# Optimization experiments

Measured on AMD Instinct MI355X. Metric: run time of the kernel, lower is better.

## Reference

```python
import jax, jax.numpy as jnp
import numpy as np

FEAT_DIM = 2048
NUM_CLASSES = 1000
BATCH = 8192
REACH_SCALE = 10.0
COS_SCALE = 16.0


def setup_inputs() -> dict:
    key = jax.random.key(0)
    ks = jax.random.split(key, 7)
    x = jax.random.normal(ks[0], (BATCH, FEAT_DIM), dtype=jnp.float32)
    centroids = jax.random.normal(ks[1], (NUM_CLASSES, FEAT_DIM), dtype=jnp.float32)
    # nn.Linear-style params (W: [out, in], b: [out]), small init scale
    s_h = 1.0 / np.sqrt(FEAT_DIM)
    W_hall = jax.random.uniform(ks[2], (NUM_CLASSES, FEAT_DIM), jnp.float32, -s_h, s_h)
    b_hall = jax.random.uniform(ks[3], (NUM_CLASSES,), jnp.float32, -s_h, s_h)
    W_sel = jax.random.uniform(ks[4], (FEAT_DIM, FEAT_DIM), jnp.float32, -s_h, s_h)
    b_sel = jax.random.uniform(ks[5], (FEAT_DIM,), jnp.float32, -s_h, s_h)
    # CosNorm_Classifier weight: [num_classes, feat_dim]
    W_cos = jax.random.uniform(ks[6], (NUM_CLASSES, FEAT_DIM), jnp.float32, -s_h, s_h)
    return {"x": x, "centroids": centroids, "W_hall": W_hall, "b_hall": b_hall,
            "W_sel": W_sel, "b_sel": b_sel, "W_cos": W_cos}


def reference(x, centroids, W_hall, b_hall, W_sel, b_sel, W_cos):
    # --- min Euclidean distance to centroids via the matmul identity ---
    x_sq = jnp.sum(x * x, axis=1, keepdims=True)               # [B, 1]
    c_sq = jnp.sum(centroids * centroids, axis=1)[None, :]     # [1, C]
    d2 = x_sq + c_sq - 2.0 * (x @ centroids.T)                 # [B, C]
    min_dist = jnp.sqrt(jnp.maximum(jnp.min(d2, axis=1), 0.0)) # [B]
    reachability = (REACH_SCALE / min_dist)[:, None]           # [B, 1] (broadcasts over feat)

    # --- hallucinated memory attention over class centroids ---
    values_memory = jax.nn.softmax(x @ W_hall.T + b_hall, axis=1)  # [B, C]
    memory_feature = values_memory @ centroids                     # [B, D]

    # --- gated fusion ---
    concept_selector = jnp.tanh(x @ W_sel.T + b_sel)               # [B, D]
    infused_feature = concept_selector * memory_feature            # [B, D]
    fused = reachability * (x + infused_feature)                   # [B, D]

    # --- CosNorm classifier: scale * (|x|/(1+|x|)) * (x/|x|) @ (W/|W|)^T ---
    norm_x = jnp.linalg.norm(fused, axis=1, keepdims=True)         # [B, 1]
    ex = (norm_x / (1.0 + norm_x)) * (fused / norm_x)              # [B, D]
    ew = W_cos / jnp.linalg.norm(W_cos, axis=1, keepdims=True)     # [C, D]
    logits = COS_SCALE * (ex @ ew.T)                               # [B, C]

    direct_feature = x
    return logits, direct_feature, infused_feature
```

## Files before the change

kernel.cpp:

```cpp
#include <hip/hip_runtime.h>
#include <hip/hip_bf16.h>

typedef __bf16 bf16x8 __attribute__((ext_vector_type(8)));
typedef float  f32x4  __attribute__((ext_vector_type(4)));
typedef unsigned short u16;

__device__ __forceinline__ u16 f2bf(float f) {
    __hip_bfloat16 h = __float2bfloat16(f);
    return __builtin_bit_cast(unsigned short, h);
}
__device__ __forceinline__ float bf2f(u16 u) {
    return __bfloat162float(__builtin_bit_cast(__hip_bfloat16, u));
}

template <int MODE>
__device__ __forceinline__ float blockReduce(float v, float* sbuf) {
    #pragma unroll
    for (int off = 32; off > 0; off >>= 1) {
        float o = __shfl_down(v, off, 64);
        v = (MODE == 0) ? v + o : (MODE == 1) ? fmaxf(v, o) : fminf(v, o);
    }
    int lane = threadIdx.x & 63, w = threadIdx.x >> 6;
    __syncthreads();
    if (lane == 0) sbuf[w] = v;
    __syncthreads();
    float r = sbuf[0];
    #pragma unroll
    for (int i = 1; i < 4; ++i) {
        float o = sbuf[i];
        r = (MODE == 0) ? r + o : (MODE == 1) ? fmaxf(r, o) : fminf(r, o);
    }
    return r;
}

__global__ void convert_x(const float* __restrict__ src, u16* __restrict__ dst,
                          float* __restrict__ rowsq, float* __restrict__ copyOut) {
    __shared__ float sbuf[4];
    int r = blockIdx.x, t = threadIdx.x;
    size_t base = (size_t)r * 2048 + t * 8;
    float4 a0 = *(const float4*)(src + base);
    float4 a1 = *(const float4*)(src + base + 4);
    float ss = a0.x*a0.x + a0.y*a0.y + a0.z*a0.z + a0.w*a0.w
             + a1.x*a1.x + a1.y*a1.y + a1.z*a1.z + a1.w*a1.w;
    ushort4 u0, u1;
    u0.x = f2bf(a0.x); u0.y = f2bf(a0.y); u0.z = f2bf(a0.z); u0.w = f2bf(a0.w);
    u1.x = f2bf(a1.x); u1.y = f2bf(a1.y); u1.z = f2bf(a1.z); u1.w = f2bf(a1.w);
    *(ushort4*)(dst + base)     = u0;
    *(ushort4*)(dst + base + 4) = u1;
    *(float4*)(copyOut + base)     = a0;
    *(float4*)(copyOut + base + 4) = a1;
    ss = blockReduce<0>(ss, sbuf);
    if (t == 0) rowsq[r] = ss;
}

__global__ void convert_weights(const float* __restrict__ cent, const float* __restrict__ whall,
                                const float* __restrict__ wsel, u16* __restrict__ Bp,
                                float* __restrict__ csq) {
    __shared__ float sbuf[4];
    int r = blockIdx.x, t = threadIdx.x;
    const float* src; int sr; bool valid;
    if (r < 1024)       { src = cent;  sr = r;        valid = sr < 1000; }
    else if (r < 2048)  { src = whall; sr = r - 1024; valid = sr < 1000; }
    else                { src = wsel;  sr = r - 2048; valid = true; }
    size_t dbase = (size_t)r * 2048 + t * 8;
    float ss = 0.f;
    ushort4 u0 = {0,0,0,0}, u1 = {0,0,0,0};
    if (valid) {
        size_t sbase = (size_t)sr * 2048 + t * 8;
        float4 a0 = *(const float4*)(src + sbase);
        float4 a1 = *(const float4*)(src + sbase + 4);
        ss = a0.x*a0.x + a0.y*a0.y + a0.z*a0.z + a0.w*a0.w
           + a1.x*a1.x + a1.y*a1.y + a1.z*a1.z + a1.w*a1.w;
        u0.x = f2bf(a0.x); u0.y = f2bf(a0.y); u0.z = f2bf(a0.z); u0.w = f2bf(a0.w);
        u1.x = f2bf(a1.x); u1.y = f2bf(a1.y); u1.z = f2bf(a1.z); u1.w = f2bf(a1.w);
    }
    *(ushort4*)(Bp + dbase)     = u0;
    *(ushort4*)(Bp + dbase + 4) = u1;
    if (r < 1024) {
        ss = blockReduce<0>(ss, sbuf);
        if (t == 0) csq[r] = ss;
    }
}

__global__ void norm_rows(const float* __restrict__ src, u16* __restrict__ dst, int validRows) {
    __shared__ float sbuf[4];
    int r = blockIdx.x, t = threadIdx.x;
    size_t base = (size_t)r * 2048 + t * 8;
    ushort4 u0 = {0,0,0,0}, u1 = {0,0,0,0};
    if (r < validRows) {
        float4 a0 = *(const float4*)(src + base);
        float4 a1 = *(const float4*)(src + base + 4);
        float ss = a0.x*a0.x + a0.y*a0.y + a0.z*a0.z + a0.w*a0.w
                 + a1.x*a1.x + a1.y*a1.y + a1.z*a1.z + a1.w*a1.w;
        ss = blockReduce<0>(ss, sbuf);
        float sc = 1.f / sqrtf(ss);
        u0.x = f2bf(a0.x*sc); u0.y = f2bf(a0.y*sc); u0.z = f2bf(a0.z*sc); u0.w = f2bf(a0.w*sc);
        u1.x = f2bf(a1.x*sc); u1.y = f2bf(a1.y*sc); u1.z = f2bf(a1.z*sc); u1.w = f2bf(a1.w*sc);
    }
    *(ushort4*)(dst + base)     = u0;
    *(ushort4*)(dst + base + 4) = u1;
}

__global__ void transpose_to_bf16(const float* __restrict__ src, u16* __restrict__ dst, int validRows) {
    __shared__ u16 tile[32][33];
    int d0 = blockIdx.x * 32;
    int c0 = blockIdx.y * 32;
    int tx = threadIdx.x, ty = threadIdx.y;
    #pragma unroll
    for (int k = 0; k < 4; ++k) {
        int c = c0 + ty + k * 8;
        float v = (c < validRows) ? src[(size_t)c * 2048 + d0 + tx] : 0.f;
        tile[ty + k * 8][tx] = f2bf(v);
    }
    __syncthreads();
    #pragma unroll
    for (int k = 0; k < 4; ++k) {
        int d = d0 + ty + k * 8;
        dst[(size_t)d * 1024 + c0 + tx] = tile[tx][ty + k * 8];
    }
}

template <int EPI>
__global__ __launch_bounds__(256, 4)
void gemm_bt(const u16* __restrict__ A, const u16* __restrict__ Bt,
             float* __restrict__ Cf, u16* __restrict__ Cb,
             int K, int ldc, int nValid,
             const float* __restrict__ bias,
             const u16* __restrict__ selp, int ldsel,
             const float* __restrict__ reach, const u16* __restrict__ xh2,
             u16* __restrict__ fusedh) {
    __shared__ u16 As[128 * 64];
    __shared__ u16 Bs[128 * 64];
    const int tid  = threadIdx.x;
    const int lane = tid & 63;
    const int w    = tid >> 6;
    const int wr   = w >> 1, wc = w & 1;
    const int quad = lane >> 4, r16 = lane & 15;
    const int sw   = r16 & 7;
    const int lr   = lane >> 3;
    const int lc   = lane & 7;
    const int lk   = (lc ^ lr) * 8;
    const size_t rowBase = (size_t)blockIdx.y * 128;
    const size_t colBase = (size_t)blockIdx.x * 128;

    f32x4 acc[4][4] = {};

    for (int kt = 0; kt < K; kt += 64) {
        #pragma unroll
        for (int i = 0; i < 4; ++i) {
            int ci = w * 4 + i;
            const u16* ga = A  + (rowBase + ci * 8 + lr) * (size_t)K + kt + lk;
            const u16* gb = Bt + (colBase + ci * 8 + lr) * (size_t)K + kt + lk;
            __builtin_amdgcn_global_load_lds(
                (const __attribute__((address_space(1))) void*)ga,
                (__attribute__((address_space(3))) void*)(As + ci * 512), 16, 0, 0);
            __builtin_amdgcn_global_load_lds(
                (const __attribute__((address_space(1))) void*)gb,
                (__attribute__((address_space(3))) void*)(Bs + ci * 512), 16, 0, 0);
        }
        __syncthreads();
        #pragma unroll
        for (int kk2 = 0; kk2 < 2; ++kk2) {
            const int off = (((kk2 << 2) | quad) ^ sw) * 8;
            bf16x8 a[4], b[4];
            #pragma unroll
            for (int i = 0; i < 4; ++i)
                a[i] = *(const bf16x8*)(As + (wr * 64 + i * 16 + r16) * 64 + off);
            #pragma unroll
            for (int j = 0; j < 4; ++j)
                b[j] = *(const bf16x8*)(Bs + (wc * 64 + j * 16 + r16) * 64 + off);
            #pragma unroll
            for (int i = 0; i < 4; ++i)
                #pragma unroll
                for (int j = 0; j < 4; ++j)
                    acc[i][j] = __builtin_amdgcn_mfma_f32_16x16x32_bf16(a[i], b[j], acc[i][j], 0, 0, 0);
        }
        __syncthreads();
    }

    #pragma unroll
    for (int i = 0; i < 4; ++i) {
        #pragma unroll
        for (int j = 0; j < 4; ++j) {
            #pragma unroll
            for (int v = 0; v < 4; ++v) {
                size_t grow = rowBase + wr * 64 + i * 16 + quad * 4 + v;
                size_t gcol = colBase + wc * 64 + j * 16 + r16;
                float val = acc[i][j][v];
                if (EPI == 1) {
                    Cb[grow * (size_t)ldc + gcol] = f2bf(val);
                } else if (EPI == 2) {
                    float sv  = bf2f(selp[grow * (size_t)ldsel + gcol]);
                    float t   = tanhf(sv + bias[gcol]);
                    float inf = t * val;
                    Cf[grow * (size_t)ldc + gcol] = inf;
                    float xv = bf2f(xh2[grow * (size_t)ldc + gcol]);
                    fusedh[grow * (size_t)ldc + gcol] = f2bf(reach[grow] * (xv + inf));
                } else if (EPI == 3) {
                    if ((int)gcol < nValid) Cf[grow * (size_t)ldc + gcol] = bias[grow] * val;
                }
            }
        }
    }
}

__global__ void min_softmax(const u16* __restrict__ Sp, const float* __restrict__ xsq,
                            const float* __restrict__ csq, const float* __restrict__ bh,
                            float* __restrict__ reach, u16* __restrict__ Vm) {
    __shared__ float sbuf[4];
    int r = blockIdx.x, t = threadIdx.x;
    size_t rb = (size_t)r * 4096;
    float m = 1e30f;
    for (int c = t; c < 1000; c += 256)
        m = fminf(m, csq[c] - 2.f * bf2f(Sp[rb + c]));
    m = blockReduce<2>(m, sbuf);
    if (t == 0) {
        float d2 = xsq[r] + m;
        reach[r] = 10.f / sqrtf(fmaxf(d2, 0.f));
    }
    float l[4];
    float mx = -1e30f;
    #pragma unroll
    for (int i = 0; i < 4; ++i) {
        int c = t + i * 256;
        l[i] = (c < 1000) ? (bf2f(Sp[rb + 1024 + c]) + bh[c]) : -1e30f;
        mx = fmaxf(mx, l[i]);
    }
    mx = blockReduce<1>(mx, sbuf);
    float s = 0.f;
    #pragma unroll
    for (int i = 0; i < 4; ++i) {
        int c = t + i * 256;
        l[i] = (c < 1000) ? expf(l[i] - mx) : 0.f;
        s += l[i];
    }
    s = blockReduce<0>(s, sbuf);
    float inv = 1.f / s;
    #pragma unroll
    for (int i = 0; i < 4; ++i) {
        int c = t + i * 256;
        Vm[(size_t)r * 1024 + c] = f2bf(l[i] * inv);
    }
}

__global__ void rowsq_scale(const u16* __restrict__ fusedh, float* __restrict__ scale) {
    __shared__ float sbuf[4];
    int r = blockIdx.x, t = threadIdx.x;
    size_t base = (size_t)r * 2048 + t * 8;
    ushort4 u0 = *(const ushort4*)(fusedh + base);
    ushort4 u1 = *(const ushort4*)(fusedh + base + 4);
    float f0 = bf2f(u0.x), f1 = bf2f(u0.y), f2 = bf2f(u0.z), f3 = bf2f(u0.w);
    float f4 = bf2f(u1.x), f5 = bf2f(u1.y), f6 = bf2f(u1.z), f7 = bf2f(u1.w);
    float ss = f0*f0 + f1*f1 + f2*f2 + f3*f3 + f4*f4 + f5*f5 + f6*f6 + f7*f7;
    ss = blockReduce<0>(ss, sbuf);
    if (t == 0) scale[r] = 16.f / (1.f + sqrtf(ss));
}

extern "C" void kernel_launch(void* const* d_in, const int* in_sizes, int n_in,
                              void* d_out, int out_size, void* d_ws, size_t ws_size,
                              hipStream_t stream) {
    const float* x      = (const float*)d_in[0];
    const float* cent   = (const float*)d_in[1];
    const float* W_hall = (const float*)d_in[2];
    const float* b_hall = (const float*)d_in[3];
    const float* W_sel  = (const float*)d_in[4];
    const float* b_sel  = (const float*)d_in[5];
    const float* W_cos  = (const float*)d_in[6];

    float* out_logits = (float*)d_out;
    float* out_x      = out_logits + (size_t)8192 * 1000;
    float* out_inf    = out_x      + (size_t)8192 * 2048;

    char* ws = (char*)d_ws;
    u16*   xh     = (u16*)  (ws);
    u16*   Bp     = (u16*)  (ws + 33554432);
    u16*   ew     = (u16*)  (ws + 50331648);
    u16*   centT  = (u16*)  (ws + 54525952);
    u16*   Sp     = (u16*)  (ws + 58720256);
    u16*   Vm     = (u16*)  (ws + 125829120);
    u16*   fusedh = (u16*)  (ws + 142606336);
    float* xsq    = (float*)(ws + 176160768);
    float* csq    = (float*)(ws + 176193536);
    float* reach  = (float*)(ws + 176197632);
    float* scale  = (float*)(ws + 176230400);

    (void)in_sizes; (void)n_in; (void)out_size; (void)ws_size;

    convert_x<<<8192, 256, 0, stream>>>(x, xh, xsq, out_x);
    convert_weights<<<4096, 256, 0, stream>>>(cent, W_hall, W_sel, Bp, csq);
    norm_rows<<<1024, 256, 0, stream>>>(W_cos, ew, 1000);
    transpose_to_bf16<<<dim3(64, 32), dim3(32, 8), 0, stream>>>(cent, centT, 1000);

    gemm_bt<1><<<dim3(32, 64), 256, 0, stream>>>(xh, Bp, nullptr, Sp, 2048, 4096, 0,
                                                 nullptr, nullptr, 0, nullptr, nullptr, nullptr);
    min_softmax<<<8192, 256, 0, stream>>>(Sp, xsq, csq, b_hall, reach, Vm);

    gemm_bt<2><<<dim3(16, 64), 256, 0, stream>>>(Vm, centT, out_inf, nullptr, 1024, 2048, 0,
                                                 b_sel, Sp + 2048, 4096, reach, xh, fusedh);

    rowsq_scale<<<8192, 256, 0, stream>>>(fusedh, scale);

    gemm_bt<3><<<dim3(8, 64), 256, 0, stream>>>(fusedh, ew, out_logits, nullptr, 2048, 1000, 1000,
                                                scale, nullptr, 0, nullptr, nullptr, nullptr);
}
```

Measured before the change: 551.4 us.

## Add 256x256 tiled GEMM with 4-stage async LDS pipeline for first two GEMMs

Adds a new 512-thread GEMM kernel with 256x256 output tiles, a 4-deep ring of LDS buffers filled by direct global-to-LDS loads, swizzled LDS reads, and interleaved MFMA phases with priority raising. The first two GEMMs, the fused centroid/hallucination/selector projection and the memory-feature GEMM with gated epilogue, now use this kernel in place of the 128x128 one. The aim is to raise data reuse per tile and hide global load latency behind MFMA work. In exchange it uses more registers and LDS per block, and grids get smaller (512 and 256 blocks), which may hurt load balance across CUs.

```diff
diff --git a/kernel.cpp b/kernel.cpp
--- a/kernel.cpp
+++ b/kernel.cpp
@@ -117,6 +117,128 @@
     for (int k = 0; k < 4; ++k) {
         int d = d0 + ty + k * 8;
         dst[(size_t)d * 1024 + c0 + tx] = tile[tx][ty + k * 8];
+    }
+}
+
+template <int EPI>
+__global__ __launch_bounds__(512, 2)
+void gemm256(const u16* __restrict__ A, const u16* __restrict__ Bt,
+             float* __restrict__ Cf, u16* __restrict__ Cb,
+             int K, int ldc,
+             const float* __restrict__ bias,
+             const u16* __restrict__ selp, int ldsel,
+             const float* __restrict__ reach, const u16* __restrict__ xh2,
+             u16* __restrict__ fusedh) {
+    __shared__ u16 As[4][256 * 32];
+    __shared__ u16 Bs[4][256 * 32];
+
+    const int tid  = threadIdx.x;
+    const int lane = tid & 63;
+    const int w    = tid >> 6;
+    const int wr   = w >> 2;
+    const int wc   = w & 3;
+    const int quad = lane >> 4, r16 = lane & 15;
+    const int rdOff = r16 * 32 + ((quad ^ ((r16 >> 1) & 3)) * 8);
+
+    const int lr = lane >> 2;
+    const int lc = lane & 3;
+    const int skel = (lc ^ ((lr >> 1) & 3)) * 8;
+
+    const size_t rowBase = (size_t)blockIdx.y * 256;
+    const size_t colBase = (size_t)blockIdx.x * 256;
+
+    const u16* aSrc = A  + (rowBase + (size_t)(w * 16 + lr)) * K + skel;
+    const u16* bSrc = Bt + (colBase + (size_t)(w * 16 + lr)) * K + skel;
+    const int ldsRowBase = (w * 16) * 32;
+
+    const int NT = K >> 5;
+
+    f32x4 acc[8][4] = {};
+
+    auto stage = [&](const u16* srcBase, u16* ldsArr, int srcTile) {
+        #pragma unroll
+        for (int j = 0; j < 2; ++j) {
+            const u16* src = srcBase + (size_t)(j * 128) * K + srcTile * 32;
+            __builtin_amdgcn_global_load_lds(
+                (const __attribute__((address_space(1))) void*)src,
+                (__attribute__((address_space(3))) void*)(ldsArr + j * (128 * 32) + ldsRowBase),
+                16, 0, 0);
+        }
+    };
+
+    #pragma unroll
+    for (int pt = 0; pt < 3; ++pt) {
+        stage(aSrc, As[pt], pt);
+        stage(bSrc, Bs[pt], pt);
+    }
+    asm volatile("s_waitcnt vmcnt(8)" ::: "memory");
+    __builtin_amdgcn_s_barrier();
+
+    for (int t = 0; t < NT; ++t) {
+        const int bi = t & 3;
+        const int nt3 = t + 3;
+        const int sbi = nt3 & 3;
+        const int srcTile = (nt3 < NT) ? nt3 : 0;
+        bf16x8 a[4], b[4];
+
+        #pragma unroll
+        for (int fi = 0; fi < 4; ++fi)
+            a[fi] = *(const bf16x8*)&As[bi][(wr * 128 + fi * 16) * 32 + rdOff];
+        #pragma unroll
+        for (int fj = 0; fj < 4; ++fj)
+            b[fj] = *(const bf16x8*)&Bs[bi][(wc * 64 + fj * 16) * 32 + rdOff];
+        stage(aSrc, As[sbi], srcTile);
+        __builtin_amdgcn_s_barrier();
+        asm volatile("s_waitcnt lgkmcnt(0)" ::: "memory");
+        __builtin_amdgcn_sched_barrier(0);
+        __builtin_amdgcn_s_setprio(1);
+        #pragma unroll
+        for (int fi = 0; fi < 4; ++fi)
+            #pragma unroll
+            for (int fj = 0; fj < 4; ++fj)
+                acc[fi][fj] = __builtin_amdgcn_mfma_f32_16x16x32_bf16(a[fi], b[fj], acc[fi][fj], 0, 0, 0);
+        __builtin_amdgcn_s_setprio(0);
+        __builtin_amdgcn_s_barrier();
+
+        #pragma unroll
+        for (int fi = 0; fi < 4; ++fi)
+            a[fi] = *(const bf16x8*)&As[bi][(wr * 128 + 64 + fi * 16) * 32 + rdOff];
+        stage(bSrc, Bs[sbi], srcTile);
+        __builtin_amdgcn_s_barrier();
+        asm volatile("s_waitcnt lgkmcnt(0)" ::: "memory");
+        __builtin_amdgcn_sched_barrier(0);
+        __builtin_amdgcn_s_setprio(1);
+        #pragma unroll
+        for (int fi = 0; fi < 4; ++fi)
+            #pragma unroll
+            for (int fj = 0; fj < 4; ++fj)
+                acc[4 + fi][fj] = __builtin_amdgcn_mfma_f32_16x16x32_bf16(a[fi], b[fj], acc[4 + fi][fj], 0, 0, 0);
+        __builtin_amdgcn_s_setprio(0);
+        asm volatile("s_waitcnt vmcnt(6)" ::: "memory");
+        __builtin_amdgcn_s_barrier();
+    }
+
+    #pragma unroll
+    for (int i = 0; i < 8; ++i) {
+        #pragma unroll
+        for (int j = 0; j < 4; ++j) {
+            #pragma unroll
+            for (int v = 0; v < 4; ++v) {
+                size_t grow = rowBase + wr * 128 + i * 16 + quad * 4 + v;
+                size_t gcol = colBase + wc * 64 + j * 16 + r16;
+                float val = acc[i][j][v];
+                if (EPI == 1) {
+                    Cb[grow * (size_t)ldc + gcol] = f2bf(val);
+                } else if (EPI == 2) {
+                    float sv  = bf2f(selp[grow * (size_t)ldsel + gcol]);
+                    float tnh = tanhf(sv + bias[gcol]);
+                    float inf = tnh * val;
+                    Cf[grow * (size_t)ldc + gcol] = inf;
+                    float xv = bf2f(xh2[grow * (size_t)ldc + gcol]);
+                    fusedh[grow * (size_t)ldc + gcol] = f2bf(reach[grow] * (xv + inf));
+                }
+            }
+        }
     }
 }
 
@@ -291,12 +413,12 @@
     norm_rows<<<1024, 256, 0, stream>>>(W_cos, ew, 1000);
     transpose_to_bf16<<<dim3(64, 32), dim3(32, 8), 0, stream>>>(cent, centT, 1000);
 
-    gemm_bt<1><<<dim3(32, 64), 256, 0, stream>>>(xh, Bp, nullptr, Sp, 2048, 4096, 0,
+    gemm256<1><<<dim3(16, 32), 512, 0, stream>>>(xh, Bp, nullptr, Sp, 2048, 4096,
                                                  nullptr, nullptr, 0, nullptr, nullptr, nullptr);
     min_softmax<<<8192, 256, 0, stream>>>(Sp, xsq, csq, b_hall, reach, Vm);
 
-    gemm_bt<2><<<dim3(16, 64), 256, 0, stream>>>(Vm, centT, out_inf, nullptr, 1024, 2048, 0,
-                                                 b_sel, Sp + 2048, 4096, reach, xh, fusedh);
+    gemm256<2><<<dim3(8, 32), 512, 0, stream>>>(Vm, centT, out_inf, nullptr, 1024, 2048,
+                                                b_sel, Sp + 2048, 4096, reach, xh, fusedh);
 
     rowsq_scale<<<8192, 256, 0, stream>>>(fusedh, scale);
 
```

New measurement: 608.8 us. 10.4% more time.

## Fuse row-norm into GEMM epilogue, merge W_cos normalization, vectorize softmax

Applied to the files above, without the earlier changes.

The fused-feature squared norm is now accumulated in the second GEMM's epilogue with a 16-lane shuffle reduction and per-row atomicAdd. This removes the separate rowsq_scale pass that re-read the bf16 fused buffer, and the final GEMM computes 16/(1+sqrt) itself. W_cos normalization is folded into the weight conversion kernel as extra blocks, removing one launch. min_softmax now uses ushort4 vector loads and stores on 250 threads. The trade-off is float atomics, which make the row-norm sum order nondeterministic, and the norm is now taken from fp32 values rather than the rounded bf16 ones.

```diff
diff --git a/kernel.cpp b/kernel.cpp
--- a/kernel.cpp
+++ b/kernel.cpp
@@ -34,7 +34,8 @@
 }
 
 __global__ void convert_x(const float* __restrict__ src, u16* __restrict__ dst,
-                          float* __restrict__ rowsq, float* __restrict__ copyOut) {
+                          float* __restrict__ rowsq, float* __restrict__ copyOut,
+                          float* __restrict__ scaleAcc) {
     __shared__ float sbuf[4];
     int r = blockIdx.x, t = threadIdx.x;
     size_t base = (size_t)r * 2048 + t * 8;
@@ -50,14 +51,36 @@
     *(float4*)(copyOut + base)     = a0;
     *(float4*)(copyOut + base + 4) = a1;
     ss = blockReduce<0>(ss, sbuf);
-    if (t == 0) rowsq[r] = ss;
+    if (t == 0) {
+        rowsq[r] = ss;
+        scaleAcc[r] = 0.f;
+    }
 }
 
 __global__ void convert_weights(const float* __restrict__ cent, const float* __restrict__ whall,
                                 const float* __restrict__ wsel, u16* __restrict__ Bp,
-                                float* __restrict__ csq) {
+                                float* __restrict__ csq,
+                                const float* __restrict__ wcos, u16* __restrict__ ew) {
     __shared__ float sbuf[4];
     int r = blockIdx.x, t = threadIdx.x;
+    if (r >= 4096) {
+        int rr = r - 4096;
+        size_t base = (size_t)rr * 2048 + t * 8;
+        ushort4 u0 = {0,0,0,0}, u1 = {0,0,0,0};
+        if (rr < 1000) {
+            float4 a0 = *(const float4*)(wcos + base);
+            float4 a1 = *(const float4*)(wcos + base + 4);
+            float ss = a0.x*a0.x + a0.y*a0.y + a0.z*a0.z + a0.w*a0.w
+                     + a1.x*a1.x + a1.y*a1.y + a1.z*a1.z + a1.w*a1.w;
+            ss = blockReduce<0>(ss, sbuf);
+            float sc = 1.f / sqrtf(ss);
+            u0.x = f2bf(a0.x*sc); u0.y = f2bf(a0.y*sc); u0.z = f2bf(a0.z*sc); u0.w = f2bf(a0.w*sc);
+            u1.x = f2bf(a1.x*sc); u1.y = f2bf(a1.y*sc); u1.z = f2bf(a1.z*sc); u1.w = f2bf(a1.w*sc);
+        }
+        *(ushort4*)(ew + base)     = u0;
+        *(ushort4*)(ew + base + 4) = u1;
+        return;
+    }
     const float* src; int sr; bool valid;
     if (r < 1024)       { src = cent;  sr = r;        valid = sr < 1000; }
     else if (r < 2048)  { src = whall; sr = r - 1024; valid = sr < 1000; }
@@ -82,25 +105,6 @@
     }
 }
 
-__global__ void norm_rows(const float* __restrict__ src, u16* __restrict__ dst, int validRows) {
-    __shared__ float sbuf[4];
-    int r = blockIdx.x, t = threadIdx.x;
-    size_t base = (size_t)r * 2048 + t * 8;
-    ushort4 u0 = {0,0,0,0}, u1 = {0,0,0,0};
-    if (r < validRows) {
-        float4 a0 = *(const float4*)(src + base);
-        float4 a1 = *(const float4*)(src + base + 4);
-        float ss = a0.x*a0.x + a0.y*a0.y + a0.z*a0.z + a0.w*a0.w
-                 + a1.x*a1.x + a1.y*a1.y + a1.z*a1.z + a1.w*a1.w;
-        ss = blockReduce<0>(ss, sbuf);
-        float sc = 1.f / sqrtf(ss);
-        u0.x = f2bf(a0.x*sc); u0.y = f2bf(a0.y*sc); u0.z = f2bf(a0.z*sc); u0.w = f2bf(a0.w*sc);
-        u1.x = f2bf(a1.x*sc); u1.y = f2bf(a1.y*sc); u1.z = f2bf(a1.z*sc); u1.w = f2bf(a1.w*sc);
-    }
-    *(ushort4*)(dst + base)     = u0;
-    *(ushort4*)(dst + base + 4) = u1;
-}
-
 __global__ void transpose_to_bf16(const float* __restrict__ src, u16* __restrict__ dst, int validRows) {
     __shared__ u16 tile[32][33];
     int d0 = blockIdx.x * 32;
@@ -128,7 +132,7 @@
              const float* __restrict__ bias,
              const u16* __restrict__ selp, int ldsel,
              const float* __restrict__ reach, const u16* __restrict__ xh2,
-             u16* __restrict__ fusedh) {
+             u16* __restrict__ fusedh, float* __restrict__ scaleAcc) {
     __shared__ u16 As[128 * 64];
     __shared__ u16 Bs[128 * 64];
     const int tid  = threadIdx.x;
@@ -178,26 +182,51 @@
         __syncthreads();
     }
 
-    #pragma unroll
-    for (int i = 0; i < 4; ++i) {
+    if (EPI == 2) {
         #pragma unroll
-        for (int j = 0; j < 4; ++j) {
+        for (int i = 0; i < 4; ++i) {
             #pragma unroll
             for (int v = 0; v < 4; ++v) {
                 size_t grow = rowBase + wr * 64 + i * 16 + quad * 4 + v;
-                size_t gcol = colBase + wc * 64 + j * 16 + r16;
-                float val = acc[i][j][v];
-                if (EPI == 1) {
-                    Cb[grow * (size_t)ldc + gcol] = f2bf(val);
-                } else if (EPI == 2) {
+                float rch = reach[grow];
+                float rs = 0.f;
+                #pragma unroll
+                for (int j = 0; j < 4; ++j) {
+                    size_t gcol = colBase + wc * 64 + j * 16 + r16;
+                    float val = acc[i][j][v];
                     float sv  = bf2f(selp[grow * (size_t)ldsel + gcol]);
                     float t   = tanhf(sv + bias[gcol]);
                     float inf = t * val;
                     Cf[grow * (size_t)ldc + gcol] = inf;
                     float xv = bf2f(xh2[grow * (size_t)ldc + gcol]);
-                    fusedh[grow * (size_t)ldc + gcol] = f2bf(reach[grow] * (xv + inf));
-                } else if (EPI == 3) {
-                    if ((int)gcol < nValid) Cf[grow * (size_t)ldc + gcol] = bias[grow] * val;
+                    float fs = rch * (xv + inf);
+                    fusedh[grow * (size_t)ldc + gcol] = f2bf(fs);
+                    rs += fs * fs;
+                }
+                #pragma unroll
+                for (int off = 8; off > 0; off >>= 1)
+                    rs += __shfl_down(rs, off, 16);
+                if (r16 == 0) atomicAdd(&scaleAcc[grow], rs);
+            }
+        }
+    } else {
+        #pragma unroll
+        for (int i = 0; i < 4; ++i) {
+            #pragma unroll
+            for (int j = 0; j < 4; ++j) {
+                #pragma unroll
+                for (int v = 0; v < 4; ++v) {
+                    size_t grow = rowBase + wr * 64 + i * 16 + quad * 4 + v;
+                    size_t gcol = colBase + wc * 64 + j * 16 + r16;
+                    float val = acc[i][j][v];
+                    if (EPI == 1) {
+                        Cb[grow * (size_t)ldc + gcol] = f2bf(val);
+                    } else if (EPI == 3) {
+                        if ((int)gcol < nValid) {
+                            float sc = 16.f / (1.f + sqrtf(bias[grow]));
+                            Cf[grow * (size_t)ldc + gcol] = sc * val;
+                        }
+                    }
                 }
             }
         }
@@ -210,9 +239,13 @@
     __shared__ float sbuf[4];
     int r = blockIdx.x, t = threadIdx.x;
     size_t rb = (size_t)r * 4096;
+    int c0 = t * 4;
     float m = 1e30f;
-    for (int c = t; c < 1000; c += 256)
-        m = fminf(m, csq[c] - 2.f * bf2f(Sp[rb + c]));
+    if (t < 250) {
+        ushort4 d4 = *(const ushort4*)(Sp + rb + c0);
+        m = fminf(fminf(csq[c0+0] - 2.f * bf2f(d4.x), csq[c0+1] - 2.f * bf2f(d4.y)),
+                  fminf(csq[c0+2] - 2.f * bf2f(d4.z), csq[c0+3] - 2.f * bf2f(d4.w)));
+    }
     m = blockReduce<2>(m, sbuf);
     if (t == 0) {
         float d2 = xsq[r] + m;
@@ -220,40 +253,29 @@
     }
     float l[4];
     float mx = -1e30f;
-    #pragma unroll
-    for (int i = 0; i < 4; ++i) {
-        int c = t + i * 256;
-        l[i] = (c < 1000) ? (bf2f(Sp[rb + 1024 + c]) + bh[c]) : -1e30f;
-        mx = fmaxf(mx, l[i]);
+    if (t < 250) {
+        ushort4 h4 = *(const ushort4*)(Sp + rb + 1024 + c0);
+        l[0] = bf2f(h4.x) + bh[c0+0];
+        l[1] = bf2f(h4.y) + bh[c0+1];
+        l[2] = bf2f(h4.z) + bh[c0+2];
+        l[3] = bf2f(h4.w) + bh[c0+3];
+        mx = fmaxf(fmaxf(l[0], l[1]), fmaxf(l[2], l[3]));
+    } else {
+        l[0] = l[1] = l[2] = l[3] = -1e30f;
     }
     mx = blockReduce<1>(mx, sbuf);
     float s = 0.f;
     #pragma unroll
     for (int i = 0; i < 4; ++i) {
-        int c = t + i * 256;
-        l[i] = (c < 1000) ? expf(l[i] - mx) : 0.f;
+        l[i] = (t < 250) ? expf(l[i] - mx) : 0.f;
         s += l[i];
     }
     s = blockReduce<0>(s, sbuf);
     float inv = 1.f / s;
-    #pragma unroll
-    for (int i = 0; i < 4; ++i) {
-        int c = t + i * 256;
-        Vm[(size_t)r * 1024 + c] = f2bf(l[i] * inv);
-    }
-}
-
-__global__ void rowsq_scale(const u16* __restrict__ fusedh, float* __restrict__ scale) {
-    __shared__ float sbuf[4];
-    int r = blockIdx.x, t = threadIdx.x;
-    size_t base = (size_t)r * 2048 + t * 8;
-    ushort4 u0 = *(const ushort4*)(fusedh + base);
-    ushort4 u1 = *(const ushort4*)(fusedh + base + 4);
-    float f0 = bf2f(u0.x), f1 = bf2f(u0.y), f2 = bf2f(u0.z), f3 = bf2f(u0.w);
-    float f4 = bf2f(u1.x), f5 = bf2f(u1.y), f6 = bf2f(u1.z), f7 = bf2f(u1.w);
-    float ss = f0*f0 + f1*f1 + f2*f2 + f3*f3 + f4*f4 + f5*f5 + f6*f6 + f7*f7;
-    ss = blockReduce<0>(ss, sbuf);
-    if (t == 0) scale[r] = 16.f / (1.f + sqrtf(ss));
+    ushort4 o;
+    o.x = f2bf(l[0] * inv); o.y = f2bf(l[1] * inv);
+    o.z = f2bf(l[2] * inv); o.w = f2bf(l[3] * inv);
+    *(ushort4*)(Vm + (size_t)r * 1024 + c0) = o;
 }
 
 extern "C" void kernel_launch(void* const* d_in, const int* in_sizes, int n_in,
@@ -286,20 +308,17 @@
 
     (void)in_sizes; (void)n_in; (void)out_size; (void)ws_size;
 
-    convert_x<<<8192, 256, 0, stream>>>(x, xh, xsq, out_x);
-    convert_weights<<<4096, 256, 0, stream>>>(cent, W_hall, W_sel, Bp, csq);
-    norm_rows<<<1024, 256, 0, stream>>>(W_cos, ew, 1000);
+    convert_x<<<8192, 256, 0, stream>>>(x, xh, xsq, out_x, scale);
+    convert_weights<<<5120, 256, 0, stream>>>(cent, W_hall, W_sel, Bp, csq, W_cos, ew);
     transpose_to_bf16<<<dim3(64, 32), dim3(32, 8), 0, stream>>>(cent, centT, 1000);
 
     gemm_bt<1><<<dim3(32, 64), 256, 0, stream>>>(xh, Bp, nullptr, Sp, 2048, 4096, 0,
-                                                 nullptr, nullptr, 0, nullptr, nullptr, nullptr);
+                                                 nullptr, nullptr, 0, nullptr, nullptr, nullptr, nullptr);
     min_softmax<<<8192, 256, 0, stream>>>(Sp, xsq, csq, b_hall, reach, Vm);
 
     gemm_bt<2><<<dim3(16, 64), 256, 0, stream>>>(Vm, centT, out_inf, nullptr, 1024, 2048, 0,
-                                                 b_sel, Sp + 2048, 4096, reach, xh, fusedh);
-
-    rowsq_scale<<<8192, 256, 0, stream>>>(fusedh, scale);
+                                                 b_sel, Sp + 2048, 4096, reach, xh, fusedh, scale);
 
     gemm_bt<3><<<dim3(8, 64), 256, 0, stream>>>(fusedh, ew, out_logits, nullptr, 2048, 1000, 1000,
-                                                scale, nullptr, 0, nullptr, nullptr, nullptr);
-}
+                                                scale, nullptr, 0, nullptr, nullptr, nullptr, nullptr);
+}
```

Result: faster. 516.8 us (-6.3%).
